# Kernel tuning notes

Measured on AMD Instinct MI355X. Metric: run time of the kernel, lower is better.

## Reference

```python
import jax, jax.numpy as jnp
import numpy as np

N, H, W, K = 4, 512, 512, 8
V, F = 50000, 100000
SIGMA, GAMMA = 1e-4, 1e-4
ZNEAR, ZFAR = 1.0, 100.0
EPS = 1e-10


def setup_inputs() -> dict:
    key = jax.random.key(0)
    k1, k2, k3, k4, k5, k6 = jax.random.split(key, 6)
    vn = jax.random.normal(k1, (V, 3), dtype=jnp.float32)
    verts_normals = vn / jnp.linalg.norm(vn, axis=-1, keepdims=True)
    bary = jax.random.uniform(k2, (N, H, W, K, 3), dtype=jnp.float32)
    bary_coords = bary / bary.sum(-1, keepdims=True)  # valid barycentrics
    dists = jax.random.normal(k3, (N, H, W, K), dtype=jnp.float32) * 1e-4
    zbuf = jax.random.uniform(k4, (N, H, W, K), dtype=jnp.float32) * (ZFAR - ZNEAR) + ZNEAR
    faces = jax.random.randint(k5, (F, 3), 0, V, dtype=jnp.int64)
    # include -1 entries (background pixels), as in real rasterizer output
    pix_to_face = jax.random.randint(k6, (N, H, W, K), -1, F, dtype=jnp.int64)
    return {"verts_normals": verts_normals, "bary_coords": bary_coords,
            "dists": dists, "zbuf": zbuf, "faces": faces,
            "pix_to_face": pix_to_face}


def reference(verts_normals, bary_coords, dists, zbuf, faces, pix_to_face):
    # --- normal_shading: gather + barycentric interpolation of vertex normals ---
    faces_normals = verts_normals[faces]                      # (F, 3verts, 3)
    mask = pix_to_face >= 0                                   # (N,H,W,K)
    idx = jnp.where(mask, pix_to_face, 0)
    attrs = faces_normals[idx]                                # (N,H,W,K,3verts,3)
    colors = jnp.einsum('nhwkv,nhwkvc->nhwkc', bary_coords, attrs)
    colors = colors * mask[..., None]                         # zero masked pixels
    opacity = jnp.ones(mask.shape, dtype=colors.dtype)        # torch.ones_like
    # --- softmax_rgb_blend ---
    maskf = mask.astype(colors.dtype)
    prob_map = jax.nn.sigmoid(-dists / SIGMA) * maskf
    alpha = jnp.prod(1.0 - prob_map, axis=-1)                 # (N,H,W)
    z_inv = (ZFAR - zbuf) / (ZFAR - ZNEAR) * maskf
    z_inv_max = jnp.max(z_inv, axis=-1, keepdims=True)
    weights_num = prob_map * jnp.exp((z_inv - z_inv_max) / GAMMA) * opacity
    delta = jnp.maximum(jnp.exp((EPS - z_inv_max) / GAMMA), EPS)
    denom = weights_num.sum(-1, keepdims=True) + delta        # (N,H,W,1)
    background = jnp.array([1.0, 1.0, 1.0], dtype=colors.dtype)
    weighted_colors = jnp.einsum('nhwk,nhwkc->nhwc', weights_num, colors)
    rgb = (weighted_colors + delta * background) / denom      # (N,H,W,3)
    a = (1.0 - alpha)[..., None]                              # (N,H,W,1)
    return jnp.concatenate([rgb, a], axis=-1)                 # (N,H,W,4)
```

## Files before the change

kernel.cpp:

```cpp
#include <hip/hip_runtime.h>


constexpr int   N_PIX      = 4 * 512 * 512;
constexpr int   N_FRAG     = N_PIX * 8;
constexpr float INV_SIGMA  = 1.0f / 1e-4f;
constexpr float INV_GAMMA  = 1.0f / 1e-4f;
constexpr float ZFARV      = 100.0f;
constexpr float INV_ZRANGE = 1.0f / 99.0f;
constexpr float EPSV       = 1e-10f;

__global__ __launch_bounds__(256)
void build_face_normals_kernel(const float* __restrict__ vn,
                               const int*   __restrict__ faces,
                               float*       __restrict__ fn,
                               int nf)
{
    int f = blockIdx.x * blockDim.x + threadIdx.x;
    if (f >= nf) return;
    int v0 = faces[3 * f + 0];
    int v1 = faces[3 * f + 1];
    int v2 = faces[3 * f + 2];
    const float* p0 = vn + 3 * (size_t)v0;
    const float* p1 = vn + 3 * (size_t)v1;
    const float* p2 = vn + 3 * (size_t)v2;
    float4 r0 = make_float4(p0[0], p0[1], p0[2], p1[0]);
    float4 r1 = make_float4(p1[1], p1[2], p2[0], p2[1]);
    float4 r2 = make_float4(p2[2], 0.f, 0.f, 0.f);
    float4* dst = reinterpret_cast<float4*>(fn + 12 * (size_t)f);
    dst[0] = r0; dst[1] = r1; dst[2] = r2;
}

__global__ __launch_bounds__(256)
void shade_kernel(const float* __restrict__ bary,
                  const float* __restrict__ dists,
                  const float* __restrict__ zbuf,
                  const int*   __restrict__ p2f,
                  const float* __restrict__ fn,
                  const float* __restrict__ vn,
                  const int*   __restrict__ faces,
                  float*       __restrict__ out)
{
    int gid = blockIdx.x * blockDim.x + threadIdx.x;
    if (gid >= N_FRAG) return;
    int kk  = gid & 7;
    int pix = gid >> 3;

    float d  = dists[gid];
    float zb = zbuf[gid];
    int   f  = p2f[gid];

    bool  m  = f >= 0;
    float pr = m ? __builtin_amdgcn_rcpf(1.0f + __expf(d * INV_SIGMA)) : 0.0f;
    float zi = m ? (ZFARV - zb) * INV_ZRANGE : 0.0f;

    float zmax = zi;
    zmax = fmaxf(zmax, __shfl_xor(zmax, 1));
    zmax = fmaxf(zmax, __shfl_xor(zmax, 2));
    zmax = fmaxf(zmax, __shfl_xor(zmax, 4));

    float am = 1.0f - pr;
    am *= __shfl_xor(am, 1);
    am *= __shfl_xor(am, 2);
    am *= __shfl_xor(am, 4);

    float w = pr * __expf((zi - zmax) * INV_GAMMA);

    float cr = 0.0f, cg = 0.0f, cb = 0.0f;
    if (w != 0.0f) {
        float b0 = bary[3 * (size_t)gid + 0];
        float b1 = bary[3 * (size_t)gid + 1];
        float b2 = bary[3 * (size_t)gid + 2];
        float n0x, n0y, n0z, n1x, n1y, n1z, n2x, n2y, n2z;
        if (fn) {
            const float4* fr = reinterpret_cast<const float4*>(fn + 12 * (size_t)f);
            float4 r0 = fr[0], r1 = fr[1], r2 = fr[2];
            n0x = r0.x; n0y = r0.y; n0z = r0.z;
            n1x = r0.w; n1y = r1.x; n1z = r1.y;
            n2x = r1.z; n2y = r1.w; n2z = r2.x;
        } else {
            int v0 = faces[3 * f + 0];
            int v1 = faces[3 * f + 1];
            int v2 = faces[3 * f + 2];
            n0x = vn[3 * v0 + 0]; n0y = vn[3 * v0 + 1]; n0z = vn[3 * v0 + 2];
            n1x = vn[3 * v1 + 0]; n1y = vn[3 * v1 + 1]; n1z = vn[3 * v1 + 2];
            n2x = vn[3 * v2 + 0]; n2y = vn[3 * v2 + 1]; n2z = vn[3 * v2 + 2];
        }
        cr = w * (b0 * n0x + b1 * n1x + b2 * n2x);
        cg = w * (b0 * n0y + b1 * n1y + b2 * n2y);
        cb = w * (b0 * n0z + b1 * n1z + b2 * n2z);
    }

    float ws = w;
    ws += __shfl_xor(ws, 1);  cr += __shfl_xor(cr, 1);
    cg += __shfl_xor(cg, 1);  cb += __shfl_xor(cb, 1);
    ws += __shfl_xor(ws, 2);  cr += __shfl_xor(cr, 2);
    cg += __shfl_xor(cg, 2);  cb += __shfl_xor(cb, 2);
    ws += __shfl_xor(ws, 4);  cr += __shfl_xor(cr, 4);
    cg += __shfl_xor(cg, 4);  cb += __shfl_xor(cb, 4);

    if (kk == 0) {
        float delta     = fmaxf(__expf((EPSV - zmax) * INV_GAMMA), EPSV);
        float inv_denom = __builtin_amdgcn_rcpf(ws + delta);
        float4 o;
        o.x = (cr + delta) * inv_denom;
        o.y = (cg + delta) * inv_denom;
        o.z = (cb + delta) * inv_denom;
        o.w = 1.0f - am;
        reinterpret_cast<float4*>(out)[pix] = o;
    }
}

extern "C" void kernel_launch(void* const* d_in, const int* in_sizes, int n_in,
                              void* d_out, int out_size, void* d_ws, size_t ws_size,
                              hipStream_t stream) {
    const float* vn    = (const float*)d_in[0];
    const float* bary  = (const float*)d_in[1];
    const float* dists = (const float*)d_in[2];
    const float* zbuf  = (const float*)d_in[3];
    const int*   faces = (const int*)d_in[4];
    const int*   p2f   = (const int*)d_in[5];
    float*       out   = (float*)d_out;

    int nf = in_sizes[4] / 3;

    float* fn = nullptr;
    size_t need = (size_t)nf * 12 * sizeof(float);
    if (ws_size >= need) {
        fn = (float*)d_ws;
        build_face_normals_kernel<<<(nf + 255) / 256, 256, 0, stream>>>(vn, faces, fn, nf);
    }

    shade_kernel<<<N_FRAG / 256, 256, 0, stream>>>(bary, dists, zbuf, p2f,
                                                   fn, vn, faces, out);
}
```

Baseline: 228.2 us.

## Process four fragments per thread with vectorized loads, two threads per pixel

Each thread now handles four of a pixel's eight fragments. It loads dists, zbuf and pix_to_face as float4/int4 and reduces within the thread before a single shuffle step, instead of using one thread per fragment with three shuffle levels. This cuts the thread count fourfold, widens memory accesses and removes most cross-lane shuffles. The trade-off is fewer waves to hide latency on the scattered face-normal gathers, and the bary loads are no longer coalesced per lane.

After: 234.0 us. +2.6%, slower.

```diff
diff --git a/kernel.cpp b/kernel.cpp
--- a/kernel.cpp
+++ b/kernel.cpp
@@ -2,7 +2,6 @@
 
 
 constexpr int   N_PIX      = 4 * 512 * 512;
-constexpr int   N_FRAG     = N_PIX * 8;
 constexpr float INV_SIGMA  = 1.0f / 1e-4f;
 constexpr float INV_GAMMA  = 1.0f / 1e-4f;
 constexpr float ZFARV      = 100.0f;
@@ -41,64 +40,70 @@
                   float*       __restrict__ out)
 {
     int gid = blockIdx.x * blockDim.x + threadIdx.x;
-    if (gid >= N_FRAG) return;
-    int kk  = gid & 7;
-    int pix = gid >> 3;
+    int h   = gid & 1;
+    int pix = gid >> 1;
+    if (pix >= N_PIX) return;
 
-    float d  = dists[gid];
-    float zb = zbuf[gid];
-    int   f  = p2f[gid];
+    float4 d4 = reinterpret_cast<const float4*>(dists)[gid];
+    float4 z4 = reinterpret_cast<const float4*>(zbuf)[gid];
+    int4   f4 = reinterpret_cast<const int4*>(p2f)[gid];
 
-    bool  m  = f >= 0;
-    float pr = m ? __builtin_amdgcn_rcpf(1.0f + __expf(d * INV_SIGMA)) : 0.0f;
-    float zi = m ? (ZFARV - zb) * INV_ZRANGE : 0.0f;
+    float dk[4] = {d4.x, d4.y, d4.z, d4.w};
+    float zk[4] = {z4.x, z4.y, z4.z, z4.w};
+    int   fk[4] = {f4.x, f4.y, f4.z, f4.w};
 
-    float zmax = zi;
-    zmax = fmaxf(zmax, __shfl_xor(zmax, 1));
-    zmax = fmaxf(zmax, __shfl_xor(zmax, 2));
-    zmax = fmaxf(zmax, __shfl_xor(zmax, 4));
-
-    float am = 1.0f - pr;
-    am *= __shfl_xor(am, 1);
-    am *= __shfl_xor(am, 2);
-    am *= __shfl_xor(am, 4);
-
-    float w = pr * __expf((zi - zmax) * INV_GAMMA);
-
-    float cr = 0.0f, cg = 0.0f, cb = 0.0f;
-    if (w != 0.0f) {
-        float b0 = bary[3 * (size_t)gid + 0];
-        float b1 = bary[3 * (size_t)gid + 1];
-        float b2 = bary[3 * (size_t)gid + 2];
-        float n0x, n0y, n0z, n1x, n1y, n1z, n2x, n2y, n2z;
-        if (fn) {
-            const float4* fr = reinterpret_cast<const float4*>(fn + 12 * (size_t)f);
-            float4 r0 = fr[0], r1 = fr[1], r2 = fr[2];
-            n0x = r0.x; n0y = r0.y; n0z = r0.z;
-            n1x = r0.w; n1y = r1.x; n1z = r1.y;
-            n2x = r1.z; n2y = r1.w; n2z = r2.x;
-        } else {
-            int v0 = faces[3 * f + 0];
-            int v1 = faces[3 * f + 1];
-            int v2 = faces[3 * f + 2];
-            n0x = vn[3 * v0 + 0]; n0y = vn[3 * v0 + 1]; n0z = vn[3 * v0 + 2];
-            n1x = vn[3 * v1 + 0]; n1y = vn[3 * v1 + 1]; n1z = vn[3 * v1 + 2];
-            n2x = vn[3 * v2 + 0]; n2y = vn[3 * v2 + 1]; n2z = vn[3 * v2 + 2];
-        }
-        cr = w * (b0 * n0x + b1 * n1x + b2 * n2x);
-        cg = w * (b0 * n0y + b1 * n1y + b2 * n2y);
-        cb = w * (b0 * n0z + b1 * n1z + b2 * n2z);
+    float pr[4], zi[4];
+#pragma unroll
+    for (int k = 0; k < 4; ++k) {
+        bool m = fk[k] >= 0;
+        pr[k] = m ? __builtin_amdgcn_rcpf(1.0f + __expf(dk[k] * INV_SIGMA)) : 0.0f;
+        zi[k] = m ? (ZFARV - zk[k]) * INV_ZRANGE : 0.0f;
     }
 
-    float ws = w;
-    ws += __shfl_xor(ws, 1);  cr += __shfl_xor(cr, 1);
-    cg += __shfl_xor(cg, 1);  cb += __shfl_xor(cb, 1);
-    ws += __shfl_xor(ws, 2);  cr += __shfl_xor(cr, 2);
-    cg += __shfl_xor(cg, 2);  cb += __shfl_xor(cb, 2);
-    ws += __shfl_xor(ws, 4);  cr += __shfl_xor(cr, 4);
-    cg += __shfl_xor(cg, 4);  cb += __shfl_xor(cb, 4);
+    float zmax = fmaxf(fmaxf(zi[0], zi[1]), fmaxf(zi[2], zi[3]));
+    zmax = fmaxf(zmax, __shfl_xor(zmax, 1));
 
-    if (kk == 0) {
+    float am = (1.0f - pr[0]) * (1.0f - pr[1]) * (1.0f - pr[2]) * (1.0f - pr[3]);
+    am *= __shfl_xor(am, 1);
+
+    float ws = 0.0f, cr = 0.0f, cg = 0.0f, cb = 0.0f;
+#pragma unroll
+    for (int k = 0; k < 4; ++k) {
+        float w = pr[k] * __expf((zi[k] - zmax) * INV_GAMMA);
+        ws += w;
+        if (w != 0.0f) {
+            int f = fk[k];
+            size_t bo = 12 * (size_t)gid + 3 * k;
+            float b0 = bary[bo + 0];
+            float b1 = bary[bo + 1];
+            float b2 = bary[bo + 2];
+            float n0x, n0y, n0z, n1x, n1y, n1z, n2x, n2y, n2z;
+            if (fn) {
+                const float4* frp = reinterpret_cast<const float4*>(fn + 12 * (size_t)f);
+                float4 r0 = frp[0], r1 = frp[1], r2 = frp[2];
+                n0x = r0.x; n0y = r0.y; n0z = r0.z;
+                n1x = r0.w; n1y = r1.x; n1z = r1.y;
+                n2x = r1.z; n2y = r1.w; n2z = r2.x;
+            } else {
+                int v0 = faces[3 * f + 0];
+                int v1 = faces[3 * f + 1];
+                int v2 = faces[3 * f + 2];
+                n0x = vn[3 * v0 + 0]; n0y = vn[3 * v0 + 1]; n0z = vn[3 * v0 + 2];
+                n1x = vn[3 * v1 + 0]; n1y = vn[3 * v1 + 1]; n1z = vn[3 * v1 + 2];
+                n2x = vn[3 * v2 + 0]; n2y = vn[3 * v2 + 1]; n2z = vn[3 * v2 + 2];
+            }
+            cr += w * (b0 * n0x + b1 * n1x + b2 * n2x);
+            cg += w * (b0 * n0y + b1 * n1y + b2 * n2y);
+            cb += w * (b0 * n0z + b1 * n1z + b2 * n2z);
+        }
+    }
+
+    ws += __shfl_xor(ws, 1);
+    cr += __shfl_xor(cr, 1);
+    cg += __shfl_xor(cg, 1);
+    cb += __shfl_xor(cb, 1);
+
+    if (h == 0) {
         float delta     = fmaxf(__expf((EPSV - zmax) * INV_GAMMA), EPSV);
         float inv_denom = __builtin_amdgcn_rcpf(ws + delta);
         float4 o;
@@ -130,6 +135,7 @@
         build_face_normals_kernel<<<(nf + 255) / 256, 256, 0, stream>>>(vn, faces, fn, nf);
     }
 
-    shade_kernel<<<N_FRAG / 256, 256, 0, stream>>>(bary, dists, zbuf, p2f,
-                                                   fn, vn, faces, out);
+    int threads = N_PIX * 2;
+    shade_kernel<<<threads / 256, 256, 0, stream>>>(bary, dists, zbuf, p2f,
+                                                    fn, vn, faces, out);
 }
```

## Store face normals as fp16 and use a persistent grid-stride loop with prefetch

Applied to the files above, without the earlier changes.

The face-normal table is now stored as 16 halves (32 bytes per face) instead of 12 floats, which shrinks the random-gather footprint. The shade kernel runs a fixed grid of 2048 blocks in a grid-stride loop and prefetches the next iteration's dists, zbuf, pix_to_face and barycentrics. The normal gather is now unconditional, clamped to face 0 when the weight is zero, which removes the branch. In exchange, normals lose precision to fp16, the workspace-size fallback is dropped, and barycentrics are loaded even for masked fragments.

Result: no change. 232.7 us (+2.0%).

```diff
diff --git a/kernel.cpp b/kernel.cpp
--- a/kernel.cpp
+++ b/kernel.cpp
@@ -1,8 +1,12 @@
 #include <hip/hip_runtime.h>
+#include <hip/hip_fp16.h>
 
 
 constexpr int   N_PIX      = 4 * 512 * 512;
 constexpr int   N_FRAG     = N_PIX * 8;
+constexpr int   N_BLOCKS   = 2048;
+constexpr int   N_THREADS  = N_BLOCKS * 256;
+constexpr int   N_ITERS    = N_FRAG / N_THREADS;
 constexpr float INV_SIGMA  = 1.0f / 1e-4f;
 constexpr float INV_GAMMA  = 1.0f / 1e-4f;
 constexpr float ZFARV      = 100.0f;
@@ -12,7 +16,7 @@
 __global__ __launch_bounds__(256)
 void build_face_normals_kernel(const float* __restrict__ vn,
                                const int*   __restrict__ faces,
-                               float*       __restrict__ fn,
+                               __half*      __restrict__ fnh,
                                int nf)
 {
     int f = blockIdx.x * blockDim.x + threadIdx.x;
@@ -20,93 +24,108 @@
     int v0 = faces[3 * f + 0];
     int v1 = faces[3 * f + 1];
     int v2 = faces[3 * f + 2];
-    const float* p0 = vn + 3 * (size_t)v0;
-    const float* p1 = vn + 3 * (size_t)v1;
-    const float* p2 = vn + 3 * (size_t)v2;
-    float4 r0 = make_float4(p0[0], p0[1], p0[2], p1[0]);
-    float4 r1 = make_float4(p1[1], p1[2], p2[0], p2[1]);
-    float4 r2 = make_float4(p2[2], 0.f, 0.f, 0.f);
-    float4* dst = reinterpret_cast<float4*>(fn + 12 * (size_t)f);
-    dst[0] = r0; dst[1] = r1; dst[2] = r2;
+    union { ushort us[16]; uint4 u4[2]; } row;
+    row.us[0] = __half_as_ushort(__float2half(vn[3 * v0 + 0]));
+    row.us[1] = __half_as_ushort(__float2half(vn[3 * v0 + 1]));
+    row.us[2] = __half_as_ushort(__float2half(vn[3 * v0 + 2]));
+    row.us[3] = __half_as_ushort(__float2half(vn[3 * v1 + 0]));
+    row.us[4] = __half_as_ushort(__float2half(vn[3 * v1 + 1]));
+    row.us[5] = __half_as_ushort(__float2half(vn[3 * v1 + 2]));
+    row.us[6] = __half_as_ushort(__float2half(vn[3 * v2 + 0]));
+    row.us[7] = __half_as_ushort(__float2half(vn[3 * v2 + 1]));
+    row.us[8] = __half_as_ushort(__float2half(vn[3 * v2 + 2]));
+    row.us[9] = 0; row.us[10] = 0; row.us[11] = 0;
+    row.us[12] = 0; row.us[13] = 0; row.us[14] = 0; row.us[15] = 0;
+    uint4* dst = reinterpret_cast<uint4*>(fnh + 16 * (size_t)f);
+    dst[0] = row.u4[0];
+    dst[1] = row.u4[1];
 }
 
-__global__ __launch_bounds__(256)
-void shade_kernel(const float* __restrict__ bary,
-                  const float* __restrict__ dists,
-                  const float* __restrict__ zbuf,
-                  const int*   __restrict__ p2f,
-                  const float* __restrict__ fn,
-                  const float* __restrict__ vn,
-                  const int*   __restrict__ faces,
-                  float*       __restrict__ out)
+__global__ __launch_bounds__(256, 8)
+void shade_kernel(const float*  __restrict__ bary,
+                  const float*  __restrict__ dists,
+                  const float*  __restrict__ zbuf,
+                  const int*    __restrict__ p2f,
+                  const __half* __restrict__ fnh,
+                  float*        __restrict__ out)
 {
-    int gid = blockIdx.x * blockDim.x + threadIdx.x;
-    if (gid >= N_FRAG) return;
-    int kk  = gid & 7;
-    int pix = gid >> 3;
+    int gid = blockIdx.x * 256 + threadIdx.x;
+    int kk  = threadIdx.x & 7;
 
-    float d  = dists[gid];
-    float zb = zbuf[gid];
-    int   f  = p2f[gid];
+    float nd  = dists[gid];
+    float nz  = zbuf[gid];
+    int   nf_ = p2f[gid];
+    size_t nbo = 3 * (size_t)gid;
+    float nb0 = bary[nbo + 0];
+    float nb1 = bary[nbo + 1];
+    float nb2 = bary[nbo + 2];
 
-    bool  m  = f >= 0;
-    float pr = m ? __builtin_amdgcn_rcpf(1.0f + __expf(d * INV_SIGMA)) : 0.0f;
-    float zi = m ? (ZFARV - zb) * INV_ZRANGE : 0.0f;
+#pragma unroll
+    for (int it = 0; it < N_ITERS; ++it) {
+        float d  = nd, zb = nz;
+        int   f  = nf_;
+        float b0 = nb0, b1 = nb1, b2 = nb2;
 
-    float zmax = zi;
-    zmax = fmaxf(zmax, __shfl_xor(zmax, 1));
-    zmax = fmaxf(zmax, __shfl_xor(zmax, 2));
-    zmax = fmaxf(zmax, __shfl_xor(zmax, 4));
+        int gn = gid + N_THREADS;
+        if (it + 1 < N_ITERS) {
+            nd  = dists[gn];
+            nz  = zbuf[gn];
+            nf_ = p2f[gn];
+            size_t bo = 3 * (size_t)gn;
+            nb0 = bary[bo + 0];
+            nb1 = bary[bo + 1];
+            nb2 = bary[bo + 2];
+        }
 
-    float am = 1.0f - pr;
-    am *= __shfl_xor(am, 1);
-    am *= __shfl_xor(am, 2);
-    am *= __shfl_xor(am, 4);
+        bool  m  = f >= 0;
+        float pr = m ? __builtin_amdgcn_rcpf(1.0f + __expf(d * INV_SIGMA)) : 0.0f;
+        float zi = m ? (ZFARV - zb) * INV_ZRANGE : 0.0f;
 
-    float w = pr * __expf((zi - zmax) * INV_GAMMA);
+        float zmax = zi;
+        zmax = fmaxf(zmax, __shfl_xor(zmax, 1));
+        zmax = fmaxf(zmax, __shfl_xor(zmax, 2));
+        zmax = fmaxf(zmax, __shfl_xor(zmax, 4));
 
-    float cr = 0.0f, cg = 0.0f, cb = 0.0f;
-    if (w != 0.0f) {
-        float b0 = bary[3 * (size_t)gid + 0];
-        float b1 = bary[3 * (size_t)gid + 1];
-        float b2 = bary[3 * (size_t)gid + 2];
-        float n0x, n0y, n0z, n1x, n1y, n1z, n2x, n2y, n2z;
-        if (fn) {
-            const float4* fr = reinterpret_cast<const float4*>(fn + 12 * (size_t)f);
-            float4 r0 = fr[0], r1 = fr[1], r2 = fr[2];
-            n0x = r0.x; n0y = r0.y; n0z = r0.z;
-            n1x = r0.w; n1y = r1.x; n1z = r1.y;
-            n2x = r1.z; n2y = r1.w; n2z = r2.x;
-        } else {
-            int v0 = faces[3 * f + 0];
-            int v1 = faces[3 * f + 1];
-            int v2 = faces[3 * f + 2];
-            n0x = vn[3 * v0 + 0]; n0y = vn[3 * v0 + 1]; n0z = vn[3 * v0 + 2];
-            n1x = vn[3 * v1 + 0]; n1y = vn[3 * v1 + 1]; n1z = vn[3 * v1 + 2];
-            n2x = vn[3 * v2 + 0]; n2y = vn[3 * v2 + 1]; n2z = vn[3 * v2 + 2];
+        float am = 1.0f - pr;
+        am *= __shfl_xor(am, 1);
+        am *= __shfl_xor(am, 2);
+        am *= __shfl_xor(am, 4);
+
+        float w  = pr * __expf((zi - zmax) * INV_GAMMA);
+        int   fe = (w != 0.0f) ? f : 0;
+
+        const __half* hp = fnh + 16 * (size_t)fe;
+        uint4 a  = *reinterpret_cast<const uint4*>(hp);
+        uint  b8 = reinterpret_cast<const uint*>(hp)[4];
+        float2 q0 = __half22float2(*reinterpret_cast<const __half2*>(&a.x));
+        float2 q1 = __half22float2(*reinterpret_cast<const __half2*>(&a.y));
+        float2 q2 = __half22float2(*reinterpret_cast<const __half2*>(&a.z));
+        float2 q3 = __half22float2(*reinterpret_cast<const __half2*>(&a.w));
+        float2 q4 = __half22float2(*reinterpret_cast<const __half2*>(&b8));
+
+        float cr = w * (b0 * q0.x + b1 * q1.y + b2 * q3.x);
+        float cg = w * (b0 * q0.y + b1 * q2.x + b2 * q3.y);
+        float cb = w * (b0 * q1.x + b1 * q2.y + b2 * q4.x);
+        float ws = w;
+
+        ws += __shfl_xor(ws, 1);  cr += __shfl_xor(cr, 1);
+        cg += __shfl_xor(cg, 1);  cb += __shfl_xor(cb, 1);
+        ws += __shfl_xor(ws, 2);  cr += __shfl_xor(cr, 2);
+        cg += __shfl_xor(cg, 2);  cb += __shfl_xor(cb, 2);
+        ws += __shfl_xor(ws, 4);  cr += __shfl_xor(cr, 4);
+        cg += __shfl_xor(cg, 4);  cb += __shfl_xor(cb, 4);
+
+        if (kk == 0) {
+            float delta     = fmaxf(__expf((EPSV - zmax) * INV_GAMMA), EPSV);
+            float inv_denom = __builtin_amdgcn_rcpf(ws + delta);
+            float4 o;
+            o.x = (cr + delta) * inv_denom;
+            o.y = (cg + delta) * inv_denom;
+            o.z = (cb + delta) * inv_denom;
+            o.w = 1.0f - am;
+            reinterpret_cast<float4*>(out)[gid >> 3] = o;
         }
-        cr = w * (b0 * n0x + b1 * n1x + b2 * n2x);
-        cg = w * (b0 * n0y + b1 * n1y + b2 * n2y);
-        cb = w * (b0 * n0z + b1 * n1z + b2 * n2z);
-    }
-
-    float ws = w;
-    ws += __shfl_xor(ws, 1);  cr += __shfl_xor(cr, 1);
-    cg += __shfl_xor(cg, 1);  cb += __shfl_xor(cb, 1);
-    ws += __shfl_xor(ws, 2);  cr += __shfl_xor(cr, 2);
-    cg += __shfl_xor(cg, 2);  cb += __shfl_xor(cb, 2);
-    ws += __shfl_xor(ws, 4);  cr += __shfl_xor(cr, 4);
-    cg += __shfl_xor(cg, 4);  cb += __shfl_xor(cb, 4);
-
-    if (kk == 0) {
-        float delta     = fmaxf(__expf((EPSV - zmax) * INV_GAMMA), EPSV);
-        float inv_denom = __builtin_amdgcn_rcpf(ws + delta);
-        float4 o;
-        o.x = (cr + delta) * inv_denom;
-        o.y = (cg + delta) * inv_denom;
-        o.z = (cb + delta) * inv_denom;
-        o.w = 1.0f - am;
-        reinterpret_cast<float4*>(out)[pix] = o;
+        gid = gn;
     }
 }
 
@@ -122,14 +141,8 @@
     float*       out   = (float*)d_out;
 
     int nf = in_sizes[4] / 3;
+    __half* fnh = (__half*)d_ws;
 
-    float* fn = nullptr;
-    size_t need = (size_t)nf * 12 * sizeof(float);
-    if (ws_size >= need) {
-        fn = (float*)d_ws;
-        build_face_normals_kernel<<<(nf + 255) / 256, 256, 0, stream>>>(vn, faces, fn, nf);
-    }
-
-    shade_kernel<<<N_FRAG / 256, 256, 0, stream>>>(bary, dists, zbuf, p2f,
-                                                   fn, vn, faces, out);
+    build_face_normals_kernel<<<(nf + 255) / 256, 256, 0, stream>>>(vn, faces, fnh, nf);
+    shade_kernel<<<N_BLOCKS, 256, 0, stream>>>(bary, dists, zbuf, p2f, fnh, out);
 }
```
